# Kernel optimization log

Hardware: AMD Instinct MI355X
Metric: run time of the kernel (lower is better)

Reference implementation:

```python
import jax, jax.numpy as jnp
import numpy as np

B, N, M = 8192, 4096, 256


def setup_inputs() -> dict:
    key = jax.random.key(0)
    k_x, k_keep, k_w1, k_b1, k_w2, k_b2 = jax.random.split(key, 6)
    x = jax.random.normal(k_x, (B, N), dtype=jnp.float32)
    keep = jax.random.uniform(k_keep, (B, N)) < 0.5
    x = jnp.where(keep, x, 0.0)
    # Linear params, PyTorch-style fan-in scaling
    W1 = jax.random.normal(k_w1, (N, M), dtype=jnp.float32) / np.sqrt(N)
    b1 = jax.random.normal(k_b1, (M,), dtype=jnp.float32) * 0.01
    W2 = jax.random.normal(k_w2, (M, N), dtype=jnp.float32) / np.sqrt(M)
    b2 = jax.random.normal(k_b2, (N,), dtype=jnp.float32) * 0.01
    return {"x": x, "W1": W1, "b1": b1, "W2": W2, "b2": b2}


def reference(x, W1, b1, W2, b2):
    # f2(relu(f1(x)))
    f = jax.nn.relu(x @ W1 + b1) @ W2 + b2  # [B, N]
    mask = x != 0
    # per-row sum over masked positions (vectorized version of the Python loop)
    s = jnp.sum(jnp.where(mask, f, 0.0), axis=1, keepdims=True)  # [B, 1]
    # rows with empty mask stay all-zero; guard divide-by-zero for those rows
    s_safe = jnp.where(s == 0.0, 1.0, s)
    y = jnp.where(mask, f / s_safe, 0.0)
    return y
```

## Files before the change

### kernel.cpp

```cpp
#include <hip/hip_runtime.h>

typedef _Float16 f16;
typedef __fp16 h16x2 __attribute__((ext_vector_type(2)));
typedef _Float16 f16x8 __attribute__((ext_vector_type(8)));
typedef float f32x4 __attribute__((ext_vector_type(4)));

#define MFMA16(a,b,c) __builtin_amdgcn_mfma_f32_16x16x32_f16((a),(b),(c),0,0,0)

__device__ __forceinline__ void gload16(const void* g, void* l) {
  __builtin_amdgcn_global_load_lds(
      (const __attribute__((address_space(1))) void*)g,
      (__attribute__((address_space(3))) void*)l, 16, 0, 0);
}

__device__ __forceinline__ int swz(int r, int c) {
  return r * 32 + ((c ^ (r & 3)) << 3);
}

__device__ __forceinline__ void split8(const f32x4 v0, const f32x4 v1,
                                       f16x8& hv, f16x8& lv) {
  h16x2 h01 = __builtin_amdgcn_cvt_pkrtz(v0[0], v0[1]);
  h16x2 h23 = __builtin_amdgcn_cvt_pkrtz(v0[2], v0[3]);
  h16x2 h45 = __builtin_amdgcn_cvt_pkrtz(v1[0], v1[1]);
  h16x2 h67 = __builtin_amdgcn_cvt_pkrtz(v1[2], v1[3]);
  hv[0] = (f16)h01[0]; hv[1] = (f16)h01[1]; hv[2] = (f16)h23[0]; hv[3] = (f16)h23[1];
  hv[4] = (f16)h45[0]; hv[5] = (f16)h45[1]; hv[6] = (f16)h67[0]; hv[7] = (f16)h67[1];
  h16x2 l01 = __builtin_amdgcn_cvt_pkrtz(v0[0] - (float)h01[0], v0[1] - (float)h01[1]);
  h16x2 l23 = __builtin_amdgcn_cvt_pkrtz(v0[2] - (float)h23[0], v0[3] - (float)h23[1]);
  h16x2 l45 = __builtin_amdgcn_cvt_pkrtz(v1[0] - (float)h45[0], v1[1] - (float)h45[1]);
  h16x2 l67 = __builtin_amdgcn_cvt_pkrtz(v1[2] - (float)h67[0], v1[3] - (float)h67[1]);
  lv[0] = (f16)l01[0]; lv[1] = (f16)l01[1]; lv[2] = (f16)l23[0]; lv[3] = (f16)l23[1];
  lv[4] = (f16)l45[0]; lv[5] = (f16)l45[1]; lv[6] = (f16)l67[0]; lv[7] = (f16)l67[1];
}

__global__ __launch_bounds__(256) void k_prep(const float* __restrict__ in,
                                              f16* __restrict__ oh, f16* __restrict__ ol,
                                              int R, int C) {
  __shared__ float t[64][65];
  int c0 = blockIdx.x * 64, r0 = blockIdx.y * 64;
  int tid = threadIdx.x;
#pragma unroll
  for (int i = 0; i < 16; ++i) {
    int idx = tid + i * 256;
    int r = idx >> 6, c = idx & 63;
    t[r][c] = in[(size_t)(r0 + r) * C + (c0 + c)];
  }
  __syncthreads();
  int tiles_per_col = R >> 5;
#pragma unroll
  for (int w = 0; w < 2; ++w) {
    int idx = tid + w * 256;
    int kt = idx >> 8, rr = (idx >> 2) & 63, cc = idx & 3;
    f32x4 v0, v1;
#pragma unroll
    for (int j = 0; j < 4; ++j) v0[j] = t[kt * 32 + cc * 8 + j][rr];
#pragma unroll
    for (int j = 0; j < 4; ++j) v1[j] = t[kt * 32 + cc * 8 + 4 + j][rr];
    f16x8 hv, lv;
    split8(v0, v1, hv, lv);
    size_t tileIdx = (size_t)(c0 >> 6) * tiles_per_col + (r0 >> 5) + kt;
    size_t off = tileIdx * 2048 + swz(rr, cc);
    *(f16x8*)&oh[off] = hv;
    *(f16x8*)&ol[off] = lv;
  }
}

__global__ __launch_bounds__(256, 4) void k_gemm1(
    const float* __restrict__ X, const f16* __restrict__ Bht,
    const f16* __restrict__ Blt, unsigned char* __restrict__ mb,
    float* __restrict__ partials) {
  __shared__ f16 sm[2][4][64 * 32];
  int m0 = blockIdx.x * 64, nb = blockIdx.y, kc = blockIdx.z;
  int tid = threadIdx.x;
  int wv = tid >> 6, ln = tid & 63, lr = ln & 15, lg = ln >> 4;
  int wr = wv >> 1, wc = wv & 1;
  int ar = tid >> 2, ac = tid & 3;
  const int NS = 64;
  int kbase = kc * 2048;
  const float* xrow = X + (size_t)(m0 + ar) * 4096 + kbase + ac * 8;
  size_t btile0 = ((size_t)nb * 128 + (size_t)kc * 64) * 2048;
  bool domask = (nb == 0);
  f32x4 acc[2][2] = {};

  {
    gload16(Bht + btile0 + (size_t)tid * 8, &sm[0][2][wv * 512]);
    gload16(Blt + btile0 + (size_t)tid * 8, &sm[0][3][wv * 512]);
    f32x4 v0 = *(const f32x4*)(xrow);
    f32x4 v1 = *(const f32x4*)(xrow + 4);
    f16x8 hv, lv;
    split8(v0, v1, hv, lv);
    *(f16x8*)&sm[0][0][swz(ar, ac)] = hv;
    *(f16x8*)&sm[0][1][swz(ar, ac)] = lv;
    if (domask) {
      unsigned m = 0;
      if (v0[0] != 0.f) m |= 1u;
      if (v0[1] != 0.f) m |= 2u;
      if (v0[2] != 0.f) m |= 4u;
      if (v0[3] != 0.f) m |= 8u;
      if (v1[0] != 0.f) m |= 16u;
      if (v1[1] != 0.f) m |= 32u;
      if (v1[2] != 0.f) m |= 64u;
      if (v1[3] != 0.f) m |= 128u;
      mb[(size_t)(m0 + ar) * 512 + (kbase >> 3) + ac] = (unsigned char)m;
    }
  }
  __syncthreads();

  int cur = 0;
  for (int s = 0; s < NS; ++s) {
    bool more = (s + 1) < NS;
    f32x4 v0, v1;
    if (more) {
      size_t bt = btile0 + (size_t)(s + 1) * 2048;
      gload16(Bht + bt + (size_t)tid * 8, &sm[cur ^ 1][2][wv * 512]);
      gload16(Blt + bt + (size_t)tid * 8, &sm[cur ^ 1][3][wv * 512]);
      v0 = *(const f32x4*)(xrow + (s + 1) * 32);
      v1 = *(const f32x4*)(xrow + (s + 1) * 32 + 4);
    }
    f16x8 fah[2], fal[2], fbh[2], fbl[2];
#pragma unroll
    for (int fi = 0; fi < 2; ++fi) {
      int r = wr * 32 + fi * 16 + lr;
      fah[fi] = *(const f16x8*)&sm[cur][0][swz(r, lg)];
      fal[fi] = *(const f16x8*)&sm[cur][1][swz(r, lg)];
    }
#pragma unroll
    for (int fj = 0; fj < 2; ++fj) {
      int c = wc * 32 + fj * 16 + lr;
      fbh[fj] = *(const f16x8*)&sm[cur][2][swz(c, lg)];
      fbl[fj] = *(const f16x8*)&sm[cur][3][swz(c, lg)];
    }
#pragma unroll
    for (int fi = 0; fi < 2; ++fi)
#pragma unroll
      for (int fj = 0; fj < 2; ++fj) {
        acc[fi][fj] = MFMA16(fah[fi], fbh[fj], acc[fi][fj]);
        acc[fi][fj] = MFMA16(fah[fi], fbl[fj], acc[fi][fj]);
        acc[fi][fj] = MFMA16(fal[fi], fbh[fj], acc[fi][fj]);
      }
    if (more) {
      f16x8 hv, lv;
      split8(v0, v1, hv, lv);
      *(f16x8*)&sm[cur ^ 1][0][swz(ar, ac)] = hv;
      *(f16x8*)&sm[cur ^ 1][1][swz(ar, ac)] = lv;
      if (domask) {
        unsigned m = 0;
        if (v0[0] != 0.f) m |= 1u;
        if (v0[1] != 0.f) m |= 2u;
        if (v0[2] != 0.f) m |= 4u;
        if (v0[3] != 0.f) m |= 8u;
        if (v1[0] != 0.f) m |= 16u;
        if (v1[1] != 0.f) m |= 32u;
        if (v1[2] != 0.f) m |= 64u;
        if (v1[3] != 0.f) m |= 128u;
        mb[(size_t)(m0 + ar) * 512 + ((kbase + (s + 1) * 32) >> 3) + ac] =
            (unsigned char)m;
      }
    }
    __syncthreads();
    cur ^= 1;
  }

  float* pout = partials + (size_t)kc * 8192 * 256;
#pragma unroll
  for (int fi = 0; fi < 2; ++fi)
#pragma unroll
    for (int fj = 0; fj < 2; ++fj)
#pragma unroll
      for (int r = 0; r < 4; ++r) {
        int row = m0 + wr * 32 + fi * 16 + lg * 4 + r;
        int col = nb * 64 + wc * 32 + fj * 16 + lr;
        pout[(size_t)row * 256 + col] = acc[fi][fj][r];
      }
}

__global__ __launch_bounds__(256) void k_hsplit(const float* __restrict__ p,
                                                const float* __restrict__ b1,
                                                f16* __restrict__ Hh,
                                                f16* __restrict__ Hl) {
  int g = blockIdx.x * 256 + threadIdx.x;
  int r = g >> 5, c = g & 31;
  const float* p0 = p + (size_t)r * 256 + c * 8;
  const float* p1 = p0 + (size_t)8192 * 256;
  f32x4 a0 = *(const f32x4*)p0, a1 = *(const f32x4*)(p0 + 4);
  f32x4 d0 = *(const f32x4*)p1, d1 = *(const f32x4*)(p1 + 4);
  f32x4 bb0 = *(const f32x4*)(b1 + c * 8), bb1 = *(const f32x4*)(b1 + c * 8 + 4);
  f32x4 v0, v1;
#pragma unroll
  for (int j = 0; j < 4; ++j) {
    float v = a0[j] + d0[j] + bb0[j];
    v0[j] = v > 0.f ? v : 0.f;
    float w = a1[j] + d1[j] + bb1[j];
    v1[j] = w > 0.f ? w : 0.f;
  }
  f16x8 hv, lv;
  split8(v0, v1, hv, lv);
  size_t tileIdx = (size_t)(r >> 6) * 8 + (c >> 2);
  size_t off = tileIdx * 2048 + swz(r & 63, c & 3);
  *(f16x8*)&Hh[off] = hv;
  *(f16x8*)&Hl[off] = lv;
}

__global__ __launch_bounds__(256, 4) void k_gemm2(
    const f16* __restrict__ At_h, const f16* __restrict__ At_l,
    const f16* __restrict__ Bt_h, const f16* __restrict__ Bt_l,
    const float* __restrict__ b2, const unsigned* __restrict__ maskw,
    float* __restrict__ out, float* __restrict__ partials) {
  __shared__ f16 sm[2][4][64 * 32];
  __shared__ unsigned mlds[64][2];
  __shared__ float rsum[64][2];
  int m0 = blockIdx.x * 64, n0 = blockIdx.y * 64;
  int tid = threadIdx.x;
  int wv = tid >> 6, ln = tid & 63, lr = ln & 15, lg = ln >> 4;
  int wr = wv >> 1, wc = wv & 1;
  if (tid < 128) {
    int r = tid >> 1, w = tid & 1;
    mlds[r][w] = maskw[(size_t)(m0 + r) * 128 + (n0 >> 5) + w];
  }
  size_t atile0 = (size_t)blockIdx.x * 8 * 2048;
  size_t btile0 = (size_t)blockIdx.y * 8 * 2048;
  f32x4 acc[2][2] = {};

  gload16(At_h + atile0 + (size_t)tid * 8, &sm[0][0][wv * 512]);
  gload16(At_l + atile0 + (size_t)tid * 8, &sm[0][1][wv * 512]);
  gload16(Bt_h + btile0 + (size_t)tid * 8, &sm[0][2][wv * 512]);
  gload16(Bt_l + btile0 + (size_t)tid * 8, &sm[0][3][wv * 512]);
  __syncthreads();

  int cur = 0;
  for (int s = 0; s < 8; ++s) {
    bool more = (s + 1) < 8;
    if (more) {
      size_t at = atile0 + (size_t)(s + 1) * 2048;
      size_t bt = btile0 + (size_t)(s + 1) * 2048;
      gload16(At_h + at + (size_t)tid * 8, &sm[cur ^ 1][0][wv * 512]);
      gload16(At_l + at + (size_t)tid * 8, &sm[cur ^ 1][1][wv * 512]);
      gload16(Bt_h + bt + (size_t)tid * 8, &sm[cur ^ 1][2][wv * 512]);
      gload16(Bt_l + bt + (size_t)tid * 8, &sm[cur ^ 1][3][wv * 512]);
    }
    f16x8 fah[2], fal[2], fbh[2], fbl[2];
#pragma unroll
    for (int fi = 0; fi < 2; ++fi) {
      int r = wr * 32 + fi * 16 + lr;
      fah[fi] = *(const f16x8*)&sm[cur][0][swz(r, lg)];
      fal[fi] = *(const f16x8*)&sm[cur][1][swz(r, lg)];
    }
#pragma unroll
    for (int fj = 0; fj < 2; ++fj) {
      int c = wc * 32 + fj * 16 + lr;
      fbh[fj] = *(const f16x8*)&sm[cur][2][swz(c, lg)];
      fbl[fj] = *(const f16x8*)&sm[cur][3][swz(c, lg)];
    }
#pragma unroll
    for (int fi = 0; fi < 2; ++fi)
#pragma unroll
      for (int fj = 0; fj < 2; ++fj) {
        acc[fi][fj] = MFMA16(fah[fi], fbh[fj], acc[fi][fj]);
        acc[fi][fj] = MFMA16(fah[fi], fbl[fj], acc[fi][fj]);
        acc[fi][fj] = MFMA16(fal[fi], fbh[fj], acc[fi][fj]);
      }
    __syncthreads();
    cur ^= 1;
  }

  float rp[2][4] = {};
#pragma unroll
  for (int fi = 0; fi < 2; ++fi)
#pragma unroll
    for (int fj = 0; fj < 2; ++fj)
#pragma unroll
      for (int r = 0; r < 4; ++r) {
        int row = wr * 32 + fi * 16 + lg * 4 + r;
        int col = wc * 32 + fj * 16 + lr;
        float v = acc[fi][fj][r] + b2[n0 + col];
        unsigned wd = mlds[row][col >> 5];
        float mv = ((wd >> (col & 31)) & 1u) ? v : 0.f;
        out[(size_t)(m0 + row) * 4096 + (n0 + col)] = mv;
        rp[fi][r] += mv;
      }
#pragma unroll
  for (int fi = 0; fi < 2; ++fi)
#pragma unroll
    for (int r = 0; r < 4; ++r) {
      float s = rp[fi][r];
      s += __shfl_xor(s, 1);
      s += __shfl_xor(s, 2);
      s += __shfl_xor(s, 4);
      s += __shfl_xor(s, 8);
      if (lr == 0) rsum[wr * 32 + fi * 16 + lg * 4 + r][wc] = s;
    }
  __syncthreads();
  if (tid < 64)
    partials[(size_t)(m0 + tid) * 64 + blockIdx.y] = rsum[tid][0] + rsum[tid][1];
}

__global__ __launch_bounds__(256) void k_rowinv(const float* __restrict__ partials,
                                                float* __restrict__ inv) {
  int r = blockIdx.x * 256 + threadIdx.x;
  if (r < 8192) {
    float s = 0.f;
#pragma unroll 4
    for (int i = 0; i < 64; ++i) s += partials[(size_t)r * 64 + i];
    float ss = (s == 0.f) ? 1.f : s;
    inv[r] = 1.f / ss;
  }
}

__global__ __launch_bounds__(256) void k_scale(float* __restrict__ out,
                                               const float* __restrict__ inv) {
  int v = blockIdx.x * 256 + threadIdx.x;
  float iv = inv[v >> 10];
  f32x4* p = (f32x4*)out;
  f32x4 d = p[v];
  d[0] *= iv; d[1] *= iv; d[2] *= iv; d[3] *= iv;
  p[v] = d;
}

extern "C" void kernel_launch(void* const* d_in, const int* in_sizes, int n_in,
                              void* d_out, int out_size, void* d_ws, size_t ws_size,
                              hipStream_t stream) {
  const float* x  = (const float*)d_in[0];
  const float* W1 = (const float*)d_in[1];
  const float* b1 = (const float*)d_in[2];
  const float* W2 = (const float*)d_in[3];
  const float* b2 = (const float*)d_in[4];
  float* out = (float*)d_out;
  char* ws = (char*)d_ws;

  f16* W1t_h = (f16*)(ws + ((size_t)0 << 20));
  f16* W1t_l = (f16*)(ws + ((size_t)2 << 20));
  f16* W2t_h = (f16*)(ws + ((size_t)4 << 20));
  f16* W2t_l = (f16*)(ws + ((size_t)6 << 20));
  f16* Hh    = (f16*)(ws + ((size_t)8 << 20));
  f16* Hl    = (f16*)(ws + ((size_t)12 << 20));
  unsigned char* mb = (unsigned char*)(ws + ((size_t)16 << 20));
  float* part1 = (float*)(ws + ((size_t)20 << 20));
  float* part2 = (float*)(ws + ((size_t)36 << 20));
  float* inv_s = (float*)(ws + ((size_t)38 << 20));

  k_prep<<<dim3(4, 64), 256, 0, stream>>>(W1, W1t_h, W1t_l, 4096, 256);
  k_prep<<<dim3(64, 4), 256, 0, stream>>>(W2, W2t_h, W2t_l, 256, 4096);
  k_gemm1<<<dim3(128, 4, 2), 256, 0, stream>>>(x, W1t_h, W1t_l, mb, part1);
  k_hsplit<<<1024, 256, 0, stream>>>(part1, b1, Hh, Hl);
  k_gemm2<<<dim3(128, 64), 256, 0, stream>>>(Hh, Hl, W2t_h, W2t_l, b2,
                                             (const unsigned*)mb, out, part2);
  k_rowinv<<<32, 256, 0, stream>>>(part2, inv_s);
  k_scale<<<32768, 256, 0, stream>>>(out, inv_s);
}
```

Baseline: 220.5 us.

## Pre-split X into tiled f16, pipeline GEMM1 wider, store f16 intermediate output

Adds a pre-pass that converts X into tiled hi/lo f16 buffers and the mask, so GEMM1 can stream both operands via direct LDS loads. GEMM1 gets 128-wide tiles and a three-stage pipeline. GEMM2 now writes masked values as f16, and the final scaling pass reads f16 and writes fp32. This aims to cut GEMM1's load stalls and the scale pass's memory traffic. The costs are an extra full pass over X and reduced precision of the unnormalised values. The new path only runs when the workspace is large enough.

```diff
diff --git a/kernel.cpp b/kernel.cpp
--- a/kernel.cpp
+++ b/kernel.cpp
@@ -17,8 +17,8 @@
   return r * 32 + ((c ^ (r & 3)) << 3);
 }
 
-__device__ __forceinline__ void split8(const f32x4 v0, const f32x4 v1,
-                                       f16x8& hv, f16x8& lv) {
+__device__ __forceinline__ void split8z(const f32x4 v0, const f32x4 v1,
+                                        f16x8& hv, f16x8& lv) {
   h16x2 h01 = __builtin_amdgcn_cvt_pkrtz(v0[0], v0[1]);
   h16x2 h23 = __builtin_amdgcn_cvt_pkrtz(v0[2], v0[3]);
   h16x2 h45 = __builtin_amdgcn_cvt_pkrtz(v1[0], v1[1]);
@@ -33,9 +33,18 @@
   lv[4] = (f16)l45[0]; lv[5] = (f16)l45[1]; lv[6] = (f16)l67[0]; lv[7] = (f16)l67[1];
 }
 
+__device__ __forceinline__ void split8n(const f32x4 v0, const f32x4 v1,
+                                        f16x8& hv, f16x8& lv) {
+#pragma unroll
+  for (int j = 0; j < 4; ++j) {
+    f16 h0 = (f16)v0[j]; hv[j] = h0; lv[j] = (f16)(v0[j] - (float)h0);
+    f16 h1 = (f16)v1[j]; hv[j + 4] = h1; lv[j + 4] = (f16)(v1[j] - (float)h1);
+  }
+}
+
 __global__ __launch_bounds__(256) void k_prep(const float* __restrict__ in,
                                               f16* __restrict__ oh, f16* __restrict__ ol,
-                                              int R, int C) {
+                                              int R, int C, int trShift) {
   __shared__ float t[64][65];
   int c0 = blockIdx.x * 64, r0 = blockIdx.y * 64;
   int tid = threadIdx.x;
@@ -46,26 +55,143 @@
     t[r][c] = in[(size_t)(r0 + r) * C + (c0 + c)];
   }
   __syncthreads();
-  int tiles_per_col = R >> 5;
+  int ktiles = R >> 5;
+  int TRm1 = (1 << trShift) - 1;
 #pragma unroll
   for (int w = 0; w < 2; ++w) {
     int idx = tid + w * 256;
-    int kt = idx >> 8, rr = (idx >> 2) & 63, cc = idx & 3;
+    int nn = idx >> 3, cc8 = idx & 7;
     f32x4 v0, v1;
 #pragma unroll
-    for (int j = 0; j < 4; ++j) v0[j] = t[kt * 32 + cc * 8 + j][rr];
-#pragma unroll
-    for (int j = 0; j < 4; ++j) v1[j] = t[kt * 32 + cc * 8 + 4 + j][rr];
+    for (int j = 0; j < 4; ++j) v0[j] = t[cc8 * 8 + j][nn];
+#pragma unroll
+    for (int j = 0; j < 4; ++j) v1[j] = t[cc8 * 8 + 4 + j][nn];
     f16x8 hv, lv;
-    split8(v0, v1, hv, lv);
-    size_t tileIdx = (size_t)(c0 >> 6) * tiles_per_col + (r0 >> 5) + kt;
-    size_t off = tileIdx * 2048 + swz(rr, cc);
+    split8n(v0, v1, hv, lv);
+    int gn = c0 + nn, gk = r0 + cc8 * 8;
+    size_t tileIdx = (size_t)(gn >> trShift) * ktiles + (gk >> 5);
+    size_t off = (tileIdx << (trShift + 5)) + ((size_t)(gn & TRm1) << 5) +
+                 (((cc8 & 3) ^ (gn & 3)) << 3);
     *(f16x8*)&oh[off] = hv;
     *(f16x8*)&ol[off] = lv;
   }
 }
 
-__global__ __launch_bounds__(256, 4) void k_gemm1(
+__global__ __launch_bounds__(256) void k_xprep(const float* __restrict__ X,
+                                               f16* __restrict__ Xh, f16* __restrict__ Xl,
+                                               unsigned short* __restrict__ mb2) {
+  int m0 = blockIdx.x * 64, kb0 = blockIdx.y * 64;
+  int tid = threadIdx.x;
+  int r = tid >> 2, c0 = (tid & 3) * 16;
+  const float* p = X + (size_t)(m0 + r) * 4096 + kb0 + c0;
+  f32x4 a0 = *(const f32x4*)p, a1 = *(const f32x4*)(p + 4);
+  f32x4 a2 = *(const f32x4*)(p + 8), a3 = *(const f32x4*)(p + 12);
+  f16x8 h0, l0, h1, l1;
+  split8n(a0, a1, h0, l0);
+  split8n(a2, a3, h1, l1);
+  int gk = kb0 + c0;
+  int kt = gk >> 5, cc = (gk & 31) >> 3;
+  size_t tile = (size_t)blockIdx.x * 128 + kt;
+  size_t o0 = tile * 2048 + swz(r, cc);
+  size_t o1 = tile * 2048 + swz(r, cc + 1);
+  *(f16x8*)&Xh[o0] = h0; *(f16x8*)&Xh[o1] = h1;
+  *(f16x8*)&Xl[o0] = l0; *(f16x8*)&Xl[o1] = l1;
+  unsigned m = 0;
+#pragma unroll
+  for (int j = 0; j < 4; ++j) {
+    if (a0[j] != 0.f) m |= 1u << j;
+    if (a1[j] != 0.f) m |= 1u << (4 + j);
+    if (a2[j] != 0.f) m |= 1u << (8 + j);
+    if (a3[j] != 0.f) m |= 1u << (12 + j);
+  }
+  mb2[((size_t)(m0 + r) * 512 + (gk >> 3)) >> 1] = (unsigned short)m;
+}
+
+__global__ __launch_bounds__(256, 2) void k_gemm1p(
+    const f16* __restrict__ Xh, const f16* __restrict__ Xl,
+    const f16* __restrict__ Bht, const f16* __restrict__ Blt,
+    float* __restrict__ partials) {
+  __shared__ f16 smA[3][4096];
+  __shared__ f16 smB[3][8192];
+  int bx = blockIdx.x, nb = blockIdx.y, kc = blockIdx.z;
+  int tid = threadIdx.x;
+  int wv = tid >> 6, ln = tid & 63, lr = ln & 15, lg = ln >> 4;
+  int wr = wv >> 1, wc = wv & 1;
+  const int NS = 64;
+  size_t a0 = ((size_t)bx * 128 + (size_t)kc * 64) * 2048;
+  size_t b0 = ((size_t)nb * 128 + (size_t)kc * 64) * 4096;
+
+  auto issueTile = [&](int s, int buf) {
+    const f16* ah = Xh + a0 + (size_t)s * 2048 + (size_t)tid * 8;
+    const f16* al = Xl + a0 + (size_t)s * 2048 + (size_t)tid * 8;
+    gload16(ah, &smA[buf][wv * 512]);
+    gload16(al, &smA[buf][2048 + wv * 512]);
+    const f16* bh = Bht + b0 + (size_t)s * 4096 + (size_t)tid * 8;
+    const f16* bl = Blt + b0 + (size_t)s * 4096 + (size_t)tid * 8;
+    gload16(bh, &smB[buf][wv * 512]);
+    gload16(bh + 2048, &smB[buf][2048 + wv * 512]);
+    gload16(bl, &smB[buf][4096 + wv * 512]);
+    gload16(bl + 2048, &smB[buf][6144 + wv * 512]);
+  };
+
+  f32x4 acc[2][4] = {};
+
+  issueTile(0, 0);
+  issueTile(1, 1);
+  asm volatile("s_waitcnt vmcnt(6)" ::: "memory");
+  __builtin_amdgcn_s_barrier();
+
+  int cb = 0;
+  for (int s = 0; s < NS; ++s) {
+    if (s + 2 < NS) {
+      int pb = cb + 2; if (pb >= 3) pb -= 3;
+      issueTile(s + 2, pb);
+    }
+    const f16* ab = &smA[cb][0];
+    const f16* bb = &smB[cb][0];
+    f16x8 fah[2], fal[2], fbh[4], fbl[4];
+#pragma unroll
+    for (int fi = 0; fi < 2; ++fi) {
+      int r = wr * 32 + fi * 16 + lr;
+      fah[fi] = *(const f16x8*)(ab + swz(r, lg));
+      fal[fi] = *(const f16x8*)(ab + 2048 + swz(r, lg));
+    }
+#pragma unroll
+    for (int fj = 0; fj < 4; ++fj) {
+      int c = wc * 64 + fj * 16 + lr;
+      fbh[fj] = *(const f16x8*)(bb + swz(c, lg));
+      fbl[fj] = *(const f16x8*)(bb + 4096 + swz(c, lg));
+    }
+#pragma unroll
+    for (int fi = 0; fi < 2; ++fi)
+#pragma unroll
+      for (int fj = 0; fj < 4; ++fj) {
+        acc[fi][fj] = MFMA16(fah[fi], fbh[fj], acc[fi][fj]);
+        acc[fi][fj] = MFMA16(fah[fi], fbl[fj], acc[fi][fj]);
+        acc[fi][fj] = MFMA16(fal[fi], fbh[fj], acc[fi][fj]);
+      }
+    if (s + 2 < NS)
+      asm volatile("s_waitcnt vmcnt(6)" ::: "memory");
+    else
+      asm volatile("s_waitcnt vmcnt(0)" ::: "memory");
+    __builtin_amdgcn_s_barrier();
+    cb = cb + 1; if (cb >= 3) cb -= 3;
+  }
+
+  float* pout = partials + (size_t)kc * 8192 * 256;
+#pragma unroll
+  for (int fi = 0; fi < 2; ++fi)
+#pragma unroll
+    for (int fj = 0; fj < 4; ++fj)
+#pragma unroll
+      for (int r = 0; r < 4; ++r) {
+        int row = bx * 64 + wr * 32 + fi * 16 + lg * 4 + r;
+        int col = nb * 128 + wc * 64 + fj * 16 + lr;
+        pout[(size_t)row * 256 + col] = acc[fi][fj][r];
+      }
+}
+
+__global__ __launch_bounds__(256, 4) void k_gemm1f(
     const float* __restrict__ X, const f16* __restrict__ Bht,
     const f16* __restrict__ Blt, unsigned char* __restrict__ mb,
     float* __restrict__ partials) {
@@ -88,7 +214,7 @@
     f32x4 v0 = *(const f32x4*)(xrow);
     f32x4 v1 = *(const f32x4*)(xrow + 4);
     f16x8 hv, lv;
-    split8(v0, v1, hv, lv);
+    split8z(v0, v1, hv, lv);
     *(f16x8*)&sm[0][0][swz(ar, ac)] = hv;
     *(f16x8*)&sm[0][1][swz(ar, ac)] = lv;
     if (domask) {
@@ -140,7 +266,7 @@
       }
     if (more) {
       f16x8 hv, lv;
-      split8(v0, v1, hv, lv);
+      split8z(v0, v1, hv, lv);
       *(f16x8*)&sm[cur ^ 1][0][swz(ar, ac)] = hv;
       *(f16x8*)&sm[cur ^ 1][1][swz(ar, ac)] = lv;
       if (domask) {
@@ -194,18 +320,20 @@
     v1[j] = w > 0.f ? w : 0.f;
   }
   f16x8 hv, lv;
-  split8(v0, v1, hv, lv);
+  split8n(v0, v1, hv, lv);
   size_t tileIdx = (size_t)(r >> 6) * 8 + (c >> 2);
   size_t off = tileIdx * 2048 + swz(r & 63, c & 3);
   *(f16x8*)&Hh[off] = hv;
   *(f16x8*)&Hl[off] = lv;
 }
 
+template <bool F16OUT>
 __global__ __launch_bounds__(256, 4) void k_gemm2(
     const f16* __restrict__ At_h, const f16* __restrict__ At_l,
     const f16* __restrict__ Bt_h, const f16* __restrict__ Bt_l,
     const float* __restrict__ b2, const unsigned* __restrict__ maskw,
-    float* __restrict__ out, float* __restrict__ partials) {
+    float* __restrict__ out, f16* __restrict__ fout,
+    float* __restrict__ partials) {
   __shared__ f16 sm[2][4][64 * 32];
   __shared__ unsigned mlds[64][2];
   __shared__ float rsum[64][2];
@@ -275,7 +403,10 @@
         float v = acc[fi][fj][r] + b2[n0 + col];
         unsigned wd = mlds[row][col >> 5];
         float mv = ((wd >> (col & 31)) & 1u) ? v : 0.f;
-        out[(size_t)(m0 + row) * 4096 + (n0 + col)] = mv;
+        if (F16OUT)
+          fout[(size_t)(m0 + row) * 4096 + (n0 + col)] = (f16)mv;
+        else
+          out[(size_t)(m0 + row) * 4096 + (n0 + col)] = mv;
         rp[fi][r] += mv;
       }
 #pragma unroll
@@ -304,6 +435,22 @@
     float ss = (s == 0.f) ? 1.f : s;
     inv[r] = 1.f / ss;
   }
+}
+
+__global__ __launch_bounds__(256) void k_scale16(const f16* __restrict__ f,
+                                                 const float* __restrict__ inv,
+                                                 float* __restrict__ out) {
+  int v = blockIdx.x * 256 + threadIdx.x;
+  float iv = inv[v >> 9];
+  f16x8 d = *(const f16x8*)(f + (size_t)v * 8);
+  f32x4 o0, o1;
+#pragma unroll
+  for (int j = 0; j < 4; ++j) {
+    o0[j] = (float)d[j] * iv;
+    o1[j] = (float)d[4 + j] * iv;
+  }
+  *(f32x4*)(out + (size_t)v * 8) = o0;
+  *(f32x4*)(out + (size_t)v * 8 + 4) = o1;
 }
 
 __global__ __launch_bounds__(256) void k_scale(float* __restrict__ out,
@@ -327,23 +474,50 @@
   float* out = (float*)d_out;
   char* ws = (char*)d_ws;
 
-  f16* W1t_h = (f16*)(ws + ((size_t)0 << 20));
-  f16* W1t_l = (f16*)(ws + ((size_t)2 << 20));
-  f16* W2t_h = (f16*)(ws + ((size_t)4 << 20));
-  f16* W2t_l = (f16*)(ws + ((size_t)6 << 20));
-  f16* Hh    = (f16*)(ws + ((size_t)8 << 20));
-  f16* Hl    = (f16*)(ws + ((size_t)12 << 20));
-  unsigned char* mb = (unsigned char*)(ws + ((size_t)16 << 20));
-  float* part1 = (float*)(ws + ((size_t)20 << 20));
-  float* part2 = (float*)(ws + ((size_t)36 << 20));
-  float* inv_s = (float*)(ws + ((size_t)38 << 20));
-
-  k_prep<<<dim3(4, 64), 256, 0, stream>>>(W1, W1t_h, W1t_l, 4096, 256);
-  k_prep<<<dim3(64, 4), 256, 0, stream>>>(W2, W2t_h, W2t_l, 256, 4096);
-  k_gemm1<<<dim3(128, 4, 2), 256, 0, stream>>>(x, W1t_h, W1t_l, mb, part1);
-  k_hsplit<<<1024, 256, 0, stream>>>(part1, b1, Hh, Hl);
-  k_gemm2<<<dim3(128, 64), 256, 0, stream>>>(Hh, Hl, W2t_h, W2t_l, b2,
-                                             (const unsigned*)mb, out, part2);
-  k_rowinv<<<32, 256, 0, stream>>>(part2, inv_s);
-  k_scale<<<32768, 256, 0, stream>>>(out, inv_s);
-}
+  const size_t MB = (size_t)1 << 20;
+  if (ws_size >= 168 * MB) {
+    f16* W1t_h = (f16*)(ws + 0 * MB);
+    f16* W1t_l = (f16*)(ws + 2 * MB);
+    f16* W2t_h = (f16*)(ws + 4 * MB);
+    f16* W2t_l = (f16*)(ws + 6 * MB);
+    f16* Xh    = (f16*)(ws + 8 * MB);
+    f16* Xl    = (f16*)(ws + 72 * MB);
+    f16* Hh    = (f16*)(ws + 136 * MB);
+    f16* Hl    = (f16*)(ws + 140 * MB);
+    unsigned char* mb = (unsigned char*)(ws + 144 * MB);
+    float* part1 = (float*)(ws + 148 * MB);
+    float* part2 = (float*)(ws + 164 * MB);
+    float* inv_s = (float*)(ws + 166 * MB);
+    f16* fbuf = Xh;
+
+    k_prep<<<dim3(4, 64), 256, 0, stream>>>(W1, W1t_h, W1t_l, 4096, 256, 7);
+    k_prep<<<dim3(64, 4), 256, 0, stream>>>(W2, W2t_h, W2t_l, 256, 4096, 6);
+    k_xprep<<<dim3(128, 64), 256, 0, stream>>>(x, Xh, Xl, (unsigned short*)mb);
+    k_gemm1p<<<dim3(128, 2, 2), 256, 0, stream>>>(Xh, Xl, W1t_h, W1t_l, part1);
+    k_hsplit<<<1024, 256, 0, stream>>>(part1, b1, Hh, Hl);
+    k_gemm2<true><<<dim3(128, 64), 256, 0, stream>>>(
+        Hh, Hl, W2t_h, W2t_l, b2, (const unsigned*)mb, out, fbuf, part2);
+    k_rowinv<<<32, 256, 0, stream>>>(part2, inv_s);
+    k_scale16<<<16384, 256, 0, stream>>>(fbuf, inv_s, out);
+  } else {
+    f16* W1t_h = (f16*)(ws + 0 * MB);
+    f16* W1t_l = (f16*)(ws + 2 * MB);
+    f16* W2t_h = (f16*)(ws + 4 * MB);
+    f16* W2t_l = (f16*)(ws + 6 * MB);
+    f16* Hh    = (f16*)(ws + 8 * MB);
+    f16* Hl    = (f16*)(ws + 12 * MB);
+    unsigned char* mb = (unsigned char*)(ws + 16 * MB);
+    float* part1 = (float*)(ws + 20 * MB);
+    float* part2 = (float*)(ws + 36 * MB);
+    float* inv_s = (float*)(ws + 38 * MB);
+
+    k_prep<<<dim3(4, 64), 256, 0, stream>>>(W1, W1t_h, W1t_l, 4096, 256, 6);
+    k_prep<<<dim3(64, 4), 256, 0, stream>>>(W2, W2t_h, W2t_l, 256, 4096, 6);
+    k_gemm1f<<<dim3(128, 4, 2), 256, 0, stream>>>(x, W1t_h, W1t_l, mb, part1);
+    k_hsplit<<<1024, 256, 0, stream>>>(part1, b1, Hh, Hl);
+    k_gemm2<false><<<dim3(128, 64), 256, 0, stream>>>(
+        Hh, Hl, W2t_h, W2t_l, b2, (const unsigned*)mb, out, (f16*)0, part2);
+    k_rowinv<<<32, 256, 0, stream>>>(part2, inv_s);
+    k_scale<<<32768, 256, 0, stream>>>(out, inv_s);
+  }
+}
```

New measurement: 262.9 us. 19.2% more time.
